# Kernel optimization log

Hardware: AMD Instinct MI355X
Metric: run time of the kernel (lower is better)

Reference implementation:

```python
import jax, jax.numpy as jnp
from jax import lax
import numpy as np

L, N, K, D = 16, 16384, 16, 256  # levels, nodes/level, in-degree, node_dim


def setup_inputs() -> dict:
    key = jax.random.key(0)
    ks = jax.random.split(key, 6)
    x = jax.random.normal(ks[0], (L, N, D), dtype=jnp.float32)
    # predecessor indices: for each level l=1..L-1, node i has K parents in level l-1
    idx = jax.random.randint(ks[1], (L - 1, N, K), 0, N, dtype=jnp.int32)
    s = 1.0 / np.sqrt(D)
    W1 = jax.random.normal(ks[2], (D, D), dtype=jnp.float32) * s
    b1 = jax.random.normal(ks[3], (D,), dtype=jnp.float32) * s
    W2 = jax.random.normal(ks[4], (D, D), dtype=jnp.float32) * s
    b2 = jax.random.normal(ks[5], (D,), dtype=jnp.float32) * s
    return {"x": x, "idx": idx, "W1": W1, "b1": b1, "W2": W2, "b2": b2}


def reference(x, idx, W1, b1, W2, b2):
    # Topological propagation over a layered DAG (dgl.prop_nodes_topo semantics):
    # level 0 keeps its initial features (no in-edges -> node_update never fires);
    # level l>0: msg = relu(pre_layer(y_src_updated)); z = mean over in-edges;
    #            y = relu(update_layer(z)) + y_init.
    y0 = x[0]

    def step(y_prev, level_in):
        idx_l, x_l = level_in                      # [N,K] int, [N,D]
        msg = jax.nn.relu(y_prev @ W1 + b1)        # [N,D] edge-source messages
        z = jnp.mean(msg[idx_l], axis=1)           # gather [N,K,D] -> mean [N,D]
        y = jax.nn.relu(z @ W2 + b2) + x_l         # update + residual
        return y, y

    _, ys = lax.scan(step, y0, (idx, x[1:]))       # sequential over topo levels
    return jnp.concatenate([y0[None], ys], axis=0)  # [L,N,D] final ndata['y']
```

## Files before the change

### kernel.cpp

```cpp
#include <hip/hip_runtime.h>
#include <stdint.h>

#define NNODES 16384
#define DDIM   256
#define NLEV   16
#define KDEG   16

typedef _Float16 half8  __attribute__((ext_vector_type(8)));
typedef _Float16 half4_t __attribute__((ext_vector_type(4)));
typedef float    f32x4  __attribute__((ext_vector_type(4)));

__device__ __forceinline__ void async_copy16(const void* g, void* l) {
  __builtin_amdgcn_global_load_lds(
      (const __attribute__((address_space(1))) unsigned int*)(uintptr_t)g,
      (__attribute__((address_space(3))) unsigned int*)(uintptr_t)l,
      16, 0, 0);
}

__global__ __launch_bounds__(256) void convert_w_kernel(
    const float* __restrict__ W1, const float* __restrict__ W2,
    _Float16* __restrict__ W1t, _Float16* __restrict__ W2t) {
  int t = blockIdx.x * 256 + threadIdx.x;
  int k = t >> 8, n = t & 255;
  W1t[n * 256 + k] = (_Float16)W1[t];
  W2t[n * 256 + k] = (_Float16)W2[t];
}

__global__ __launch_bounds__(256) void init_kernel(
    const float* __restrict__ x0, float* __restrict__ out0,
    _Float16* __restrict__ y16) {
  size_t t = (size_t)blockIdx.x * 256 + threadIdx.x;
  f32x4 v = *(const f32x4*)(x0 + t * 4);
  *(f32x4*)(out0 + t * 4) = v;
  half4_t h;
  h[0] = (_Float16)v[0]; h[1] = (_Float16)v[1];
  h[2] = (_Float16)v[2]; h[3] = (_Float16)v[3];
  *(half4_t*)(y16 + t * 4) = h;
}

template <bool FINAL>
__global__ __launch_bounds__(256) void gemm_kernel(
    const _Float16* __restrict__ A, const _Float16* __restrict__ Wt,
    const float* __restrict__ bias, const float* __restrict__ xres,
    _Float16* __restrict__ o16, float* __restrict__ o32) {
  __shared__ __align__(16) unsigned char smem[12288];
  unsigned char* As = smem;
  unsigned char* Bs = smem + 4096;

  const int tid  = threadIdx.x;
  const int lane = tid & 63;
  const int w    = tid >> 6;
  const int wr   = w >> 1, wc = w & 1;
  const int tm   = blockIdx.x >> 1, tn = blockIdx.x & 1;

  f32x4 acc[2][4];
#pragma unroll
  for (int i = 0; i < 2; ++i)
#pragma unroll
    for (int j = 0; j < 4; ++j) acc[i][j] = (f32x4)(0.0f);

  const int a_khi = tid >> 6;
  const int a_row = tid & 63;
  const _Float16* a_src = A + (size_t)(tm * 64 + a_row) * 256 + a_khi * 8;
  const int b_o0   = tid * 16;
  const int b_khi0 = b_o0 >> 11;
  const int b_col0 = (b_o0 >> 4) & 127;
  const int b_o1   = tid * 16 + 4096;
  const int b_khi1 = b_o1 >> 11;
  const int b_col1 = (b_o1 >> 4) & 127;
  const _Float16* b_src0 = Wt + (size_t)(tn * 128 + b_col0) * 256 + b_khi0 * 8;
  const _Float16* b_src1 = Wt + (size_t)(tn * 128 + b_col1) * 256 + b_khi1 * 8;

  const int kh  = lane >> 4;
  const int r15 = lane & 15;

  for (int kt = 0; kt < 8; ++kt) {
    const int k0 = kt * 32;
    async_copy16(a_src + k0, As + tid * 16);
    async_copy16(b_src0 + k0, Bs + b_o0);
    async_copy16(b_src1 + k0, Bs + b_o1);
    __syncthreads();

    half8 af[2], bf[4];
#pragma unroll
    for (int mf = 0; mf < 2; ++mf)
      af[mf] = *(const half8*)(As + kh * 1024 + (wr * 32 + mf * 16 + r15) * 16);
#pragma unroll
    for (int nf = 0; nf < 4; ++nf)
      bf[nf] = *(const half8*)(Bs + kh * 2048 + (wc * 64 + nf * 16 + r15) * 16);
#pragma unroll
    for (int mf = 0; mf < 2; ++mf)
#pragma unroll
      for (int nf = 0; nf < 4; ++nf)
        acc[mf][nf] = __builtin_amdgcn_mfma_f32_16x16x32_f16(
            af[mf], bf[nf], acc[mf][nf], 0, 0, 0);
    __syncthreads();
  }

#pragma unroll
  for (int mf = 0; mf < 2; ++mf) {
    const int rbase = tm * 64 + wr * 32 + mf * 16 + (lane >> 4) * 4;
#pragma unroll
    for (int nf = 0; nf < 4; ++nf) {
      const int col = tn * 128 + wc * 64 + nf * 16 + (lane & 15);
      const float bv = bias[col];
#pragma unroll
      for (int j = 0; j < 4; ++j) {
        const size_t off = (size_t)(rbase + j) * 256 + col;
        float v = acc[mf][nf][j] + bv;
        v = fmaxf(v, 0.0f);
        if (FINAL) {
          float y = v + xres[off];
          o32[off] = y;
          o16[off] = (_Float16)y;
        } else {
          o16[off] = (_Float16)v;
        }
      }
    }
  }
}

__global__ __launch_bounds__(256) void gather_kernel(
    const _Float16* __restrict__ msg, const int* __restrict__ idx,
    _Float16* __restrict__ z) {
  const int tid  = threadIdx.x;
  const int node = blockIdx.x * 8 + (tid >> 5);
  const int c8   = (tid & 31) * 8;
  const int* ip  = idx + (size_t)node * KDEG;
  float acc[8] = {0, 0, 0, 0, 0, 0, 0, 0};
#pragma unroll
  for (int k = 0; k < KDEG; ++k) {
    const int r = ip[k];
    half8 v = *(const half8*)(msg + (size_t)r * 256 + c8);
#pragma unroll
    for (int j = 0; j < 8; ++j) acc[j] += (float)v[j];
  }
  half8 o;
#pragma unroll
  for (int j = 0; j < 8; ++j) o[j] = (_Float16)(acc[j] * 0.0625f);
  *(half8*)(z + (size_t)node * 256 + c8) = o;
}

extern "C" void kernel_launch(void* const* d_in, const int* in_sizes, int n_in,
                              void* d_out, int out_size, void* d_ws, size_t ws_size,
                              hipStream_t stream) {
  const float* x   = (const float*)d_in[0];
  const int*   idx = (const int*)d_in[1];
  const float* W1  = (const float*)d_in[2];
  const float* b1  = (const float*)d_in[3];
  const float* W2  = (const float*)d_in[4];
  const float* b2  = (const float*)d_in[5];
  float* out = (float*)d_out;

  char* ws = (char*)d_ws;
  _Float16* W1t = (_Float16*)(ws);
  _Float16* W2t = (_Float16*)(ws + 131072);
  _Float16* y16 = (_Float16*)(ws + 262144);
  _Float16* msg = (_Float16*)(ws + 262144 + 8388608);
  _Float16* z16 = (_Float16*)(ws + 262144 + 16777216);
  const size_t ND = (size_t)NNODES * DDIM;

  convert_w_kernel<<<dim3(256), dim3(256), 0, stream>>>(W1, W2, W1t, W2t);
  init_kernel<<<dim3(4096), dim3(256), 0, stream>>>(x, out, y16);

  for (int l = 1; l < NLEV; ++l) {
    gemm_kernel<false><<<dim3(512), dim3(256), 0, stream>>>(
        y16, W1t, b1, nullptr, msg, nullptr);
    gather_kernel<<<dim3(2048), dim3(256), 0, stream>>>(
        msg, idx + (size_t)(l - 1) * NNODES * KDEG, z16);
    gemm_kernel<true><<<dim3(512), dim3(256), 0, stream>>>(
        z16, W2t, b2, x + (size_t)l * ND, y16, out + (size_t)l * ND);
  }
}
```

Before: 1.117 ms.

## Fuse gather-mean into second GEMM and drop LDS staging from GEMMs

The neighbour gather-mean now writes its averaged rows straight into a swizzled LDS tile, and the update GEMM consumes that tile in the same kernel. This removes the z16 intermediate round trip through global memory and one launch per level. The message GEMM and the B operand of the fused kernel now read MFMA fragments directly from global memory (relying on L2 for W reuse) instead of staging through LDS with barriers. Block indices are remapped for locality. The gather phase limits overlap with the MFMA phase within each block, and the direct global fragment loads may be less efficient than staged loads.

```diff
diff --git a/kernel.cpp b/kernel.cpp
--- a/kernel.cpp
+++ b/kernel.cpp
@@ -1,21 +1,15 @@
 #include <hip/hip_runtime.h>
 #include <stdint.h>
 
-#define NNODES 16384
-#define DDIM   256
-#define NLEV   16
-#define KDEG   16
-
-typedef _Float16 half8  __attribute__((ext_vector_type(8)));
-typedef _Float16 half4_t __attribute__((ext_vector_type(4)));
-typedef float    f32x4  __attribute__((ext_vector_type(4)));
-
-__device__ __forceinline__ void async_copy16(const void* g, void* l) {
-  __builtin_amdgcn_global_load_lds(
-      (const __attribute__((address_space(1))) unsigned int*)(uintptr_t)g,
-      (__attribute__((address_space(3))) unsigned int*)(uintptr_t)l,
-      16, 0, 0);
-}
+#define NN 16384
+#define DD 256
+#define LV 16
+#define KD 16
+
+typedef _Float16 half8 __attribute__((ext_vector_type(8)));
+typedef _Float16 half4v __attribute__((ext_vector_type(4)));
+typedef float f32x4 __attribute__((ext_vector_type(4)));
+typedef int i32x4 __attribute__((ext_vector_type(4)));
 
 __global__ __launch_bounds__(256) void convert_w_kernel(
     const float* __restrict__ W1, const float* __restrict__ W2,
@@ -32,114 +26,153 @@
   size_t t = (size_t)blockIdx.x * 256 + threadIdx.x;
   f32x4 v = *(const f32x4*)(x0 + t * 4);
   *(f32x4*)(out0 + t * 4) = v;
-  half4_t h;
+  half4v h;
   h[0] = (_Float16)v[0]; h[1] = (_Float16)v[1];
   h[2] = (_Float16)v[2]; h[3] = (_Float16)v[3];
-  *(half4_t*)(y16 + t * 4) = h;
-}
-
-template <bool FINAL>
-__global__ __launch_bounds__(256) void gemm_kernel(
+  *(half4v*)(y16 + t * 4) = h;
+}
+
+__global__ __launch_bounds__(256, 2) void msg_gemm_kernel(
     const _Float16* __restrict__ A, const _Float16* __restrict__ Wt,
-    const float* __restrict__ bias, const float* __restrict__ xres,
-    _Float16* __restrict__ o16, float* __restrict__ o32) {
-  __shared__ __align__(16) unsigned char smem[12288];
-  unsigned char* As = smem;
-  unsigned char* Bs = smem + 4096;
-
-  const int tid  = threadIdx.x;
-  const int lane = tid & 63;
-  const int w    = tid >> 6;
-  const int wr   = w >> 1, wc = w & 1;
-  const int tm   = blockIdx.x >> 1, tn = blockIdx.x & 1;
+    const float* __restrict__ bias, _Float16* __restrict__ o16) {
+  const int bid = blockIdx.x;
+  const int s   = (bid & 7) * 64 + (bid >> 3);
+  const int tm  = s;
+  const int tn  = threadIdx.x >> 6;
+  const int lane = threadIdx.x & 63;
+  const int r15 = lane & 15, kh = lane >> 4;
 
   f32x4 acc[2][4];
 #pragma unroll
   for (int i = 0; i < 2; ++i)
 #pragma unroll
-    for (int j = 0; j < 4; ++j) acc[i][j] = (f32x4)(0.0f);
-
-  const int a_khi = tid >> 6;
-  const int a_row = tid & 63;
-  const _Float16* a_src = A + (size_t)(tm * 64 + a_row) * 256 + a_khi * 8;
-  const int b_o0   = tid * 16;
-  const int b_khi0 = b_o0 >> 11;
-  const int b_col0 = (b_o0 >> 4) & 127;
-  const int b_o1   = tid * 16 + 4096;
-  const int b_khi1 = b_o1 >> 11;
-  const int b_col1 = (b_o1 >> 4) & 127;
-  const _Float16* b_src0 = Wt + (size_t)(tn * 128 + b_col0) * 256 + b_khi0 * 8;
-  const _Float16* b_src1 = Wt + (size_t)(tn * 128 + b_col1) * 256 + b_khi1 * 8;
-
-  const int kh  = lane >> 4;
-  const int r15 = lane & 15;
-
+    for (int j = 0; j < 4; ++j) acc[i][j] = (f32x4)(0.f);
+
+  const _Float16* a0 = A  + (size_t)(tm * 32 + r15) * 256 + kh * 8;
+  const _Float16* b0 = Wt + (size_t)(tn * 64 + r15) * 256 + kh * 8;
+#pragma unroll
   for (int kt = 0; kt < 8; ++kt) {
-    const int k0 = kt * 32;
-    async_copy16(a_src + k0, As + tid * 16);
-    async_copy16(b_src0 + k0, Bs + b_o0);
-    async_copy16(b_src1 + k0, Bs + b_o1);
-    __syncthreads();
-
     half8 af[2], bf[4];
 #pragma unroll
     for (int mf = 0; mf < 2; ++mf)
-      af[mf] = *(const half8*)(As + kh * 1024 + (wr * 32 + mf * 16 + r15) * 16);
+      af[mf] = *(const half8*)(a0 + mf * 4096 + kt * 32);
 #pragma unroll
     for (int nf = 0; nf < 4; ++nf)
-      bf[nf] = *(const half8*)(Bs + kh * 2048 + (wc * 64 + nf * 16 + r15) * 16);
+      bf[nf] = *(const half8*)(b0 + nf * 4096 + kt * 32);
 #pragma unroll
     for (int mf = 0; mf < 2; ++mf)
 #pragma unroll
       for (int nf = 0; nf < 4; ++nf)
         acc[mf][nf] = __builtin_amdgcn_mfma_f32_16x16x32_f16(
             af[mf], bf[nf], acc[mf][nf], 0, 0, 0);
-    __syncthreads();
-  }
-
+  }
 #pragma unroll
   for (int mf = 0; mf < 2; ++mf) {
-    const int rbase = tm * 64 + wr * 32 + mf * 16 + (lane >> 4) * 4;
+    const int rbase = tm * 32 + mf * 16 + kh * 4;
 #pragma unroll
     for (int nf = 0; nf < 4; ++nf) {
-      const int col = tn * 128 + wc * 64 + nf * 16 + (lane & 15);
+      const int col = tn * 64 + nf * 16 + r15;
+      const float bv = bias[col];
+#pragma unroll
+      for (int j = 0; j < 4; ++j) {
+        float v = fmaxf(acc[mf][nf][j] + bv, 0.f);
+        o16[(size_t)(rbase + j) * 256 + col] = (_Float16)v;
+      }
+    }
+  }
+}
+
+__global__ __launch_bounds__(512, 2) void gather_gemm_kernel(
+    const _Float16* __restrict__ msg, const int* __restrict__ idxl,
+    const _Float16* __restrict__ Wt2, const float* __restrict__ bias,
+    const float* __restrict__ xres, _Float16* __restrict__ y16,
+    float* __restrict__ o32) {
+  __shared__ __align__(16) unsigned char As[16384];
+  const int bid = blockIdx.x;
+  const int s   = (bid & 7) * 64 + (bid >> 3);
+  const int tid = threadIdx.x;
+
+  {
+    const int r = tid >> 4, cc = tid & 15;
+    const int node = s * 32 + r;
+    const int* ip = idxl + (size_t)node * KD;
+    i32x4 q0 = *(const i32x4*)(ip);
+    i32x4 q1 = *(const i32x4*)(ip + 4);
+    i32x4 q2 = *(const i32x4*)(ip + 8);
+    i32x4 q3 = *(const i32x4*)(ip + 12);
+    const int pidx[16] = {q0[0], q0[1], q0[2], q0[3], q1[0], q1[1], q1[2], q1[3],
+                          q2[0], q2[1], q2[2], q2[3], q3[0], q3[1], q3[2], q3[3]};
+    float acc[16];
+#pragma unroll
+    for (int j = 0; j < 16; ++j) acc[j] = 0.f;
+#pragma unroll
+    for (int p = 0; p < 16; ++p) {
+      const _Float16* src = msg + (size_t)pidx[p] * 256 + cc * 16;
+      half8 v0 = *(const half8*)(src);
+      half8 v1 = *(const half8*)(src + 8);
+#pragma unroll
+      for (int j = 0; j < 8; ++j) {
+        acc[j] += (float)v0[j];
+        acc[8 + j] += (float)v1[j];
+      }
+    }
+    half8 h0, h1;
+#pragma unroll
+    for (int j = 0; j < 8; ++j) {
+      h0[j] = (_Float16)(acc[j] * 0.0625f);
+      h1[j] = (_Float16)(acc[8 + j] * 0.0625f);
+    }
+    const int kt = cc >> 1;
+    const int kb = (cc & 1) * 2;
+    const unsigned o0 = (unsigned)((kt * 2048 + kb * 512 + r * 16) ^ (kt << 4));
+    const unsigned o1 = (unsigned)((kt * 2048 + (kb + 1) * 512 + r * 16) ^ (kt << 4));
+    *(half8*)(As + o0) = h0;
+    *(half8*)(As + o1) = h1;
+  }
+  __syncthreads();
+
+  const int lane = tid & 63, w = tid >> 6;
+  const int r15 = lane & 15, kh = lane >> 4;
+  f32x4 acc2[2][2];
+#pragma unroll
+  for (int i = 0; i < 2; ++i)
+#pragma unroll
+    for (int j = 0; j < 2; ++j) acc2[i][j] = (f32x4)(0.f);
+
+  const _Float16* b0 = Wt2 + (size_t)(w * 32 + r15) * 256 + kh * 8;
+#pragma unroll
+  for (int kt = 0; kt < 8; ++kt) {
+    half8 af[2], bf[2];
+#pragma unroll
+    for (int mf = 0; mf < 2; ++mf)
+      af[mf] = *(const half8*)(As +
+          ((kt * 2048 + kh * 512 + (mf * 16 + r15) * 16) ^ (kt << 4)));
+#pragma unroll
+    for (int nf = 0; nf < 2; ++nf)
+      bf[nf] = *(const half8*)(b0 + nf * 4096 + kt * 32);
+#pragma unroll
+    for (int mf = 0; mf < 2; ++mf)
+#pragma unroll
+      for (int nf = 0; nf < 2; ++nf)
+        acc2[mf][nf] = __builtin_amdgcn_mfma_f32_16x16x32_f16(
+            af[mf], bf[nf], acc2[mf][nf], 0, 0, 0);
+  }
+#pragma unroll
+  for (int mf = 0; mf < 2; ++mf) {
+    const int rbase = s * 32 + mf * 16 + kh * 4;
+#pragma unroll
+    for (int nf = 0; nf < 2; ++nf) {
+      const int col = w * 32 + nf * 16 + r15;
       const float bv = bias[col];
 #pragma unroll
       for (int j = 0; j < 4; ++j) {
         const size_t off = (size_t)(rbase + j) * 256 + col;
-        float v = acc[mf][nf][j] + bv;
-        v = fmaxf(v, 0.0f);
-        if (FINAL) {
-          float y = v + xres[off];
-          o32[off] = y;
-          o16[off] = (_Float16)y;
-        } else {
-          o16[off] = (_Float16)v;
-        }
+        float v = fmaxf(acc2[mf][nf][j] + bv, 0.f) + xres[off];
+        o32[off] = v;
+        y16[off] = (_Float16)v;
       }
     }
   }
-}
-
-__global__ __launch_bounds__(256) void gather_kernel(
-    const _Float16* __restrict__ msg, const int* __restrict__ idx,
-    _Float16* __restrict__ z) {
-  const int tid  = threadIdx.x;
-  const int node = blockIdx.x * 8 + (tid >> 5);
-  const int c8   = (tid & 31) * 8;
-  const int* ip  = idx + (size_t)node * KDEG;
-  float acc[8] = {0, 0, 0, 0, 0, 0, 0, 0};
-#pragma unroll
-  for (int k = 0; k < KDEG; ++k) {
-    const int r = ip[k];
-    half8 v = *(const half8*)(msg + (size_t)r * 256 + c8);
-#pragma unroll
-    for (int j = 0; j < 8; ++j) acc[j] += (float)v[j];
-  }
-  half8 o;
-#pragma unroll
-  for (int j = 0; j < 8; ++j) o[j] = (_Float16)(acc[j] * 0.0625f);
-  *(half8*)(z + (size_t)node * 256 + c8) = o;
 }
 
 extern "C" void kernel_launch(void* const* d_in, const int* in_sizes, int n_in,
@@ -158,18 +191,15 @@
   _Float16* W2t = (_Float16*)(ws + 131072);
   _Float16* y16 = (_Float16*)(ws + 262144);
   _Float16* msg = (_Float16*)(ws + 262144 + 8388608);
-  _Float16* z16 = (_Float16*)(ws + 262144 + 16777216);
-  const size_t ND = (size_t)NNODES * DDIM;
+  const size_t ND = (size_t)NN * DD;
 
   convert_w_kernel<<<dim3(256), dim3(256), 0, stream>>>(W1, W2, W1t, W2t);
   init_kernel<<<dim3(4096), dim3(256), 0, stream>>>(x, out, y16);
 
-  for (int l = 1; l < NLEV; ++l) {
-    gemm_kernel<false><<<dim3(512), dim3(256), 0, stream>>>(
-        y16, W1t, b1, nullptr, msg, nullptr);
-    gather_kernel<<<dim3(2048), dim3(256), 0, stream>>>(
-        msg, idx + (size_t)(l - 1) * NNODES * KDEG, z16);
-    gemm_kernel<true><<<dim3(512), dim3(256), 0, stream>>>(
-        z16, W2t, b2, x + (size_t)l * ND, y16, out + (size_t)l * ND);
-  }
-}
+  for (int l = 1; l < LV; ++l) {
+    msg_gemm_kernel<<<dim3(512), dim3(256), 0, stream>>>(y16, W1t, b1, msg);
+    gather_gemm_kernel<<<dim3(512), dim3(512), 0, stream>>>(
+        msg, idx + (size_t)(l - 1) * NN * KD, W2t, b2,
+        x + (size_t)l * ND, y16, out + (size_t)l * ND);
+  }
+}
```

Measured after the change: 1.029 ms. -7.8%, faster.
